# Performance work log

Hardware: AMD Instinct MI355X
Metric: run time of the kernel (lower is better)

The kernel has to match this reference:

```python
import jax, jax.numpy as jnp
import numpy as np

B, C_IN, L = 8, 12, 4096
D = 64        # mamba_in_ch
DI = 2 * D    # d_inner (expand=2)
DS = 16       # d_state
DC = 4        # d_conv
DTR = 4       # dt_rank = ceil(D/16)
R = 10        # pixel-shuffle / upsample factor
K = 15        # big conv kernel size

def _p(key, shape, scale=0.05):
    return (jax.random.normal(key, shape) * scale).astype(jnp.float32)

def setup_inputs() -> dict:
    key = jax.random.key(0)
    ks = jax.random.split(key, 12)
    return dict(
        x=jax.random.normal(ks[0], (B, C_IN, L), jnp.float32),
        conv_in_w=_p(ks[1], (D, C_IN, K)), conv_in_b=jnp.zeros((D,), jnp.float32),
        in_proj_w=_p(ks[2], (2 * DI, D)),
        dw_conv_w=_p(ks[3], (DI, 1, DC)), dw_conv_b=jnp.zeros((DI,), jnp.float32),
        x_proj_w=_p(ks[4], (DTR + 2 * DS, DI)),
        dt_proj_w=_p(ks[5], (DI, DTR)), dt_proj_b=_p(ks[6], (DI,)),
        A_log=jnp.log(jnp.tile(jnp.arange(1, DS + 1, dtype=jnp.float32)[None, :], (DI, 1))),
        D_ssm=jnp.ones((DI,), jnp.float32),
        out_proj_w=_p(ks[7], (D, DI)),
        conv_merge_w=_p(ks[8], (D, D, K)), conv_merge_b=jnp.zeros((D,), jnp.float32),
        bn_gamma=jnp.ones((D,), jnp.float32), bn_beta=jnp.zeros((D,), jnp.float32),
        conv_ps1_w=_p(ks[9], (R * C_IN, D, K)), conv_ps1_b=jnp.zeros((R * C_IN,), jnp.float32),
    )

def conv1d(x, w, b, pad_l, pad_r, groups=1):
    out = jax.lax.conv_general_dilated(x, w, (1,), [(pad_l, pad_r)],
        dimension_numbers=('NCH', 'OIH', 'NCH'), feature_group_count=groups)
    return out + b[None, :, None]

def mamba_layer(x, in_proj_w, dw_w, dw_b, x_proj_w, dt_proj_w, dt_proj_b, A_log, D_ssm, out_proj_w):
    # x: (B, L, D)
    xz = jnp.einsum('bld,ed->ble', x, in_proj_w)          # (B,L,2*DI)
    xs, z = jnp.split(xz, 2, axis=-1)
    xc = jnp.transpose(xs, (0, 2, 1))                      # (B,DI,L)
    xc = conv1d(xc, dw_w, dw_b, DC - 1, 0, groups=DI)      # causal depthwise conv, truncated to L
    xs = jax.nn.silu(jnp.transpose(xc, (0, 2, 1)))         # (B,L,DI)
    dbl = jnp.einsum('bld,ed->ble', xs, x_proj_w)          # (B,L,DTR+2*DS)
    dt, Bm, Cm = jnp.split(dbl, [DTR, DTR + DS], axis=-1)
    dt = jax.nn.softplus(jnp.einsum('blr,dr->bld', dt, dt_proj_w) + dt_proj_b)  # (B,L,DI)
    A = -jnp.exp(A_log)                                    # (DI,DS)
    dA = jnp.exp(dt[..., None] * A)                        # (B,L,DI,DS)
    dBx = dt[..., None] * Bm[:, :, None, :] * xs[..., None]

    def step(h, inputs):
        dA_t, dBx_t, C_t = inputs                          # (B,DI,DS),(B,DI,DS),(B,DS)
        h = dA_t * h + dBx_t
        y = jnp.einsum('bds,bs->bd', h, C_t)
        return h, y

    h0 = jnp.zeros((x.shape[0], DI, DS), x.dtype)
    _, ys = jax.lax.scan(step, h0,
        (jnp.transpose(dA, (1, 0, 2, 3)), jnp.transpose(dBx, (1, 0, 2, 3)), jnp.transpose(Cm, (1, 0, 2))))
    y = jnp.transpose(ys, (1, 0, 2)) + xs * D_ssm          # (B,L,DI)
    y = y * jax.nn.silu(z)
    return jnp.einsum('bld,ed->ble', y, out_proj_w)        # (B,L,D)

def reference(x, conv_in_w, conv_in_b, in_proj_w, dw_conv_w, dw_conv_b, x_proj_w,
              dt_proj_w, dt_proj_b, A_log, D_ssm, out_proj_w,
              conv_merge_w, conv_merge_b, bn_gamma, bn_beta, conv_ps1_w, conv_ps1_b):
    pad = (K - 1) // 2
    x_in = jax.nn.leaky_relu(conv1d(x, conv_in_w, conv_in_b, pad, pad), 0.01)  # (B,64,L)
    xm = jnp.transpose(x_in, (0, 2, 1))
    xm = xm + mamba_layer(xm, in_proj_w, dw_conv_w, dw_conv_b, x_proj_w,
                          dt_proj_w, dt_proj_b, A_log, D_ssm, out_proj_w)     # n_layer=1, residual
    xm = jnp.transpose(xm, (0, 2, 1))                                          # (B,64,L)
    xmerge = conv1d(xm, conv_merge_w, conv_merge_b, pad, pad)
    mean = jnp.mean(xmerge, axis=(0, 2), keepdims=True)                        # BatchNorm1d (training stats)
    var = jnp.var(xmerge, axis=(0, 2), keepdims=True)
    xmerge = (xmerge - mean) * jax.lax.rsqrt(var + 1e-5) * bn_gamma[None, :, None] + bn_beta[None, :, None]
    xmerge = xmerge + x_in
    xp = conv1d(xmerge, conv_ps1_w, conv_ps1_b, pad, pad)                      # (B,120,L)
    # PixelShuffle1D(r=10): (B, r*Cout, L) -> (B, Cout, L*r)
    Bn, ch, Ln = xp.shape
    ps = xp.reshape(Bn, R, ch // R, Ln).transpose(0, 2, 3, 1).reshape(Bn, ch // R, Ln * R)
    # F.interpolate(x, scale_factor=10, mode='linear', align_corners=False)
    out_len = L * R
    src = jnp.maximum((jnp.arange(out_len, dtype=jnp.float32) + 0.5) / R - 0.5, 0.0)
    i0 = jnp.minimum(jnp.floor(src).astype(jnp.int32), L - 1)
    i1 = jnp.minimum(i0 + 1, L - 1)
    frac = src - i0.astype(jnp.float32)
    up = x[..., i0] * (1.0 - frac) + x[..., i1] * frac
    return ps + up
```

## Files before the change

### kernel.cpp

```cpp
#include <hip/hip_runtime.h>
#include <math.h>

#define BB 8
#define CIN 12
#define LL 4096
#define DD 64
#define DIx 128
#define DSx 16
#define RR 10
#define KK 15
#define NCH 256
#define CLEN 16
#define OUTL 40960

typedef __attribute__((ext_vector_type(8))) short s8v;
typedef __attribute__((ext_vector_type(8))) __bf16 b8v;
typedef __attribute__((ext_vector_type(4))) float f4v;
union frag_u { s8v s; b8v b; };

__device__ __forceinline__ unsigned short f2b(float f) {
    unsigned int u = __float_as_uint(f);
    u = (u + 0x7fffu + ((u >> 16) & 1u)) >> 16;
    return (unsigned short)u;
}
__device__ __forceinline__ float b2f(unsigned short h) {
    return __uint_as_float(((unsigned int)h) << 16);
}

template<int CI, int CO, int COT, bool LEAKY>
__global__ __launch_bounds__(256) void k_conv(const float* __restrict__ in,
        const float* __restrict__ w, const float* __restrict__ bias,
        float* __restrict__ out) {
    const int LT = 1024;
    int tid = threadIdx.x;
    int bid = blockIdx.x;
    const int nlt = LL / LT;
    const int ncog = CO / COT;
    int lt = bid % nlt;
    int cog = (bid / nlt) % ncog;
    int b = bid / (nlt * ncog);
    int l0 = lt * LT + tid * 4;
    int co0 = cog * COT;

    float acc[COT][4];
#pragma unroll
    for (int c = 0; c < COT; ++c) {
        float bv = bias[co0 + c];
#pragma unroll
        for (int j = 0; j < 4; ++j) acc[c][j] = bv;
    }
    for (int ci = 0; ci < CI; ++ci) {
        const float* inp = in + ((size_t)b * CI + ci) * LL;
        float in20[20];
#pragma unroll
        for (int q = 0; q < 5; ++q) {
            int gi = l0 - 8 + q * 4;
            if (gi >= 0 && gi + 3 < LL) {
                float4 v = *(const float4*)(inp + gi);
                in20[q*4+0] = v.x; in20[q*4+1] = v.y;
                in20[q*4+2] = v.z; in20[q*4+3] = v.w;
            } else {
#pragma unroll
                for (int j = 0; j < 4; ++j) {
                    int g = gi + j;
                    in20[q*4+j] = (g >= 0 && g < LL) ? inp[g] : 0.f;
                }
            }
        }
#pragma unroll
        for (int c = 0; c < COT; ++c) {
            const float* wp = w + ((size_t)(co0 + c) * CI + ci) * KK;
#pragma unroll
            for (int k = 0; k < KK; ++k) {
                float wv = wp[k];
#pragma unroll
                for (int j = 0; j < 4; ++j)
                    acc[c][j] += wv * in20[j + k + 1];
            }
        }
    }
#pragma unroll
    for (int c = 0; c < COT; ++c) {
        float r[4];
#pragma unroll
        for (int j = 0; j < 4; ++j) {
            float v = acc[c][j];
            if (LEAKY) v = (v >= 0.f) ? v : 0.01f * v;
            r[j] = v;
        }
        *(float4*)(out + ((size_t)b * CO + co0 + c) * LL + l0) =
            make_float4(r[0], r[1], r[2], r[3]);
    }
}

template<int CO_REAL, int NCOB>
__global__ __launch_bounds__(256) void k_wprep(const float* __restrict__ w,
        unsigned short* __restrict__ wp) {
    int idx = blockIdx.x * 256 + threadIdx.x;
    if (idx >= 15 * NCOB * 1024) return;
    int j = idx & 7;
    int lane = (idx >> 3) & 63;
    int cis = (idx >> 9) & 1;
    int rest = idx >> 10;
    int cob = rest % NCOB;
    int kk = rest / NCOB;
    int co = cob * 16 + (lane & 15);
    int ci = cis * 32 + ((lane >> 4) << 3) + j;
    float val = (co < CO_REAL) ? w[((size_t)co * 64 + ci) * KK + kk] : 0.f;
    wp[idx] = f2b(val);
}

template<int CO_REAL, int NCOB>
__global__ __launch_bounds__(256) void k_convmfma(
        const unsigned short* __restrict__ xt,
        const unsigned short* __restrict__ wp,
        const float* __restrict__ bias, float* __restrict__ out) {
    __shared__ unsigned short in_lds[142 * 72];
    const int NCOT = NCOB / 4;
    int tid = threadIdx.x;
    int bid = blockIdx.x;
    int lt = bid & 31;
    int cot = (bid >> 5) % NCOT;
    int b = bid / (32 * NCOT);
    int l0 = lt * 128;
#pragma unroll
    for (int i = 0; i < 5; ++i) {
        int q = i * 256 + tid;
        if (q < 1136) {
            int r = q >> 3, c8 = (q & 7) * 8;
            int gl = l0 - 7 + r;
            s8v v = {0,0,0,0,0,0,0,0};
            if (gl >= 0 && gl < LL)
                v = *(const s8v*)&xt[((size_t)b * LL + gl) * 64 + c8];
            *(s8v*)&in_lds[r * 72 + c8] = v;
        }
    }
    __syncthreads();
    int lane = tid & 63, wv = tid >> 6;
    int corow = (lane >> 4) << 2;
    f4v acc[4][2];
#pragma unroll
    for (int mt = 0; mt < 4; ++mt) {
#pragma unroll
        for (int r = 0; r < 4; ++r) {
            int co = cot * 64 + mt * 16 + corow + r;
            float bv = (co < CO_REAL) ? bias[co] : 0.f;
            acc[mt][0][r] = bv;
            acc[mt][1][r] = bv;
        }
    }
    int bcol = lane & 15;
    int cig = (lane >> 4) << 3;
    for (int k = 0; k < KK; ++k) {
#pragma unroll
        for (int cis = 0; cis < 2; ++cis) {
            frag_u a[4], bf[2];
#pragma unroll
            for (int mt = 0; mt < 4; ++mt)
                a[mt].s = *(const s8v*)&wp[((((k * NCOB + cot * 4 + mt) * 2 + cis) << 9)
                                           + (lane << 3))];
#pragma unroll
            for (int nt = 0; nt < 2; ++nt)
                bf[nt].s = *(const s8v*)&in_lds[(wv * 32 + nt * 16 + bcol + k) * 72
                                               + cis * 32 + cig];
#pragma unroll
            for (int mt = 0; mt < 4; ++mt)
#pragma unroll
                for (int nt = 0; nt < 2; ++nt)
                    acc[mt][nt] = __builtin_amdgcn_mfma_f32_16x16x32_bf16(
                        a[mt].b, bf[nt].b, acc[mt][nt], 0, 0, 0);
        }
    }
#pragma unroll
    for (int mt = 0; mt < 4; ++mt)
#pragma unroll
        for (int nt = 0; nt < 2; ++nt) {
            int l = l0 + wv * 32 + nt * 16 + bcol;
#pragma unroll
            for (int r = 0; r < 4; ++r) {
                int co = cot * 64 + mt * 16 + corow + r;
                if (co < CO_REAL)
                    out[((size_t)b * CO_REAL + co) * LL + l] = acc[mt][nt][r];
            }
        }
}

__global__ __launch_bounds__(256) void k_gemm_inproj(const float* __restrict__ A,
        const float* __restrict__ W, float* __restrict__ C) {
    __shared__ float At[64 * 132];
    __shared__ float Wt[64 * 132];
    int tid = threadIdx.x;
    int bid = blockIdx.x;
    int nb = bid & 1;
    int mb = bid >> 1;
    int row0 = mb * 128;
    int n0 = nb * 128;
    int b = row0 >> 12;
    int l0 = row0 & 4095;
#pragma unroll
    for (int it = 0; it < 8; ++it) {
        int idx = it * 256 + tid;
        int k = idx >> 5, m4 = (idx & 31) * 4;
        float4 v = *(const float4*)(A + ((size_t)b * DD + k) * LL + l0 + m4);
        *(float4*)&At[k * 132 + m4] = v;
    }
#pragma unroll
    for (int it = 0; it < 8; ++it) {
        int lin = it * 1024 + tid * 4;
        int n = lin >> 6, k = lin & 63;
        float4 v = *(const float4*)(W + (size_t)(n0 + n) * 64 + k);
        Wt[(k+0)*132 + n] = v.x; Wt[(k+1)*132 + n] = v.y;
        Wt[(k+2)*132 + n] = v.z; Wt[(k+3)*132 + n] = v.w;
    }
    __syncthreads();
    int tx = tid & 15, ty = tid >> 4;
    float acc[2][2][4][4] = {};
#pragma unroll 4
    for (int k = 0; k < 64; ++k) {
        float4 aLo = *(float4*)&At[k*132 + ty*4];
        float4 aHi = *(float4*)&At[k*132 + 64 + ty*4];
        float4 bLo = *(float4*)&Wt[k*132 + tx*4];
        float4 bHi = *(float4*)&Wt[k*132 + 64 + tx*4];
        float a0[4] = {aLo.x, aLo.y, aLo.z, aLo.w};
        float a1[4] = {aHi.x, aHi.y, aHi.z, aHi.w};
        float b0[4] = {bLo.x, bLo.y, bLo.z, bLo.w};
        float b1[4] = {bHi.x, bHi.y, bHi.z, bHi.w};
#pragma unroll
        for (int mm = 0; mm < 4; ++mm)
#pragma unroll
            for (int nn = 0; nn < 4; ++nn) {
                acc[0][0][mm][nn] += a0[mm] * b0[nn];
                acc[0][1][mm][nn] += a0[mm] * b1[nn];
                acc[1][0][mm][nn] += a1[mm] * b0[nn];
                acc[1][1][mm][nn] += a1[mm] * b1[nn];
            }
    }
#pragma unroll
    for (int qm = 0; qm < 2; ++qm)
#pragma unroll
        for (int mm = 0; mm < 4; ++mm) {
            int row = row0 + qm*64 + ty*4 + mm;
#pragma unroll
            for (int qn = 0; qn < 2; ++qn) {
                float4 v = make_float4(acc[qm][qn][mm][0], acc[qm][qn][mm][1],
                                       acc[qm][qn][mm][2], acc[qm][qn][mm][3]);
                *(float4*)(C + (size_t)row * 256 + n0 + qn*64 + tx*4) = v;
            }
        }
}

template<int NW, bool GUARD>
__global__ __launch_bounds__(256) void k_gemm64(const float* __restrict__ A,
        const float* __restrict__ W, float* __restrict__ out) {
    __shared__ float At[64 * 132];
    __shared__ float Wt[64 * 68];
    int tid = threadIdx.x;
    int row0 = blockIdx.x * 128;
    int tx = tid & 15, ty = tid >> 4;
    float acc[2][4][4] = {};
#pragma unroll
    for (int kt = 0; kt < 2; ++kt) {
        __syncthreads();
#pragma unroll
        for (int it = 0; it < 8; ++it) {
            int lin = it * 1024 + tid * 4;
            int m = lin >> 6, k = lin & 63;
            float4 v = *(const float4*)(A + (size_t)(row0 + m) * 128 + kt*64 + k);
            At[(k+0)*132 + m] = v.x; At[(k+1)*132 + m] = v.y;
            At[(k+2)*132 + m] = v.z; At[(k+3)*132 + m] = v.w;
        }
#pragma unroll
        for (int it = 0; it < 4; ++it) {
            int lin = it * 1024 + tid * 4;
            int n = lin >> 6, k = lin & 63;
            float4 v = make_float4(0.f, 0.f, 0.f, 0.f);
            if (!GUARD || n < NW)
                v = *(const float4*)(W + (size_t)n * 128 + kt*64 + k);
            Wt[(k+0)*68 + n] = v.x; Wt[(k+1)*68 + n] = v.y;
            Wt[(k+2)*68 + n] = v.z; Wt[(k+3)*68 + n] = v.w;
        }
        __syncthreads();
#pragma unroll 4
        for (int k = 0; k < 64; ++k) {
            float4 aLo = *(float4*)&At[k*132 + ty*4];
            float4 aHi = *(float4*)&At[k*132 + 64 + ty*4];
            float4 b4  = *(float4*)&Wt[k*68 + tx*4];
            float a0[4] = {aLo.x, aLo.y, aLo.z, aLo.w};
            float a1[4] = {aHi.x, aHi.y, aHi.z, aHi.w};
            float bv[4] = {b4.x, b4.y, b4.z, b4.w};
#pragma unroll
            for (int mm = 0; mm < 4; ++mm)
#pragma unroll
                for (int nn = 0; nn < 4; ++nn) {
                    acc[0][mm][nn] += a0[mm] * bv[nn];
                    acc[1][mm][nn] += a1[mm] * bv[nn];
                }
        }
    }
#pragma unroll
    for (int qm = 0; qm < 2; ++qm)
#pragma unroll
        for (int mm = 0; mm < 4; ++mm) {
            int row = row0 + qm*64 + ty*4 + mm;
            *(float4*)(out + (size_t)row * 64 + tx*4) =
                make_float4(acc[qm][mm][0], acc[qm][mm][1],
                            acc[qm][mm][2], acc[qm][mm][3]);
        }
}

__global__ __launch_bounds__(256) void k_gemm64_tr(const float* __restrict__ A,
        const float* __restrict__ W, const float* __restrict__ res,
        unsigned short* __restrict__ out) {
    __shared__ float smem[13312];
    float* At = smem;
    float* Wt = smem + 64*132;
    int tid = threadIdx.x;
    int row0 = blockIdx.x * 128;
    int tx = tid & 15, ty = tid >> 4;
    int b = row0 >> 12, l0 = row0 & 4095;
    float acc[2][4][4] = {};
#pragma unroll
    for (int kt = 0; kt < 2; ++kt) {
        __syncthreads();
#pragma unroll
        for (int it = 0; it < 8; ++it) {
            int lin = it * 1024 + tid * 4;
            int m = lin >> 6, k = lin & 63;
            float4 v = *(const float4*)(A + (size_t)(row0 + m) * 128 + kt*64 + k);
            At[(k+0)*132 + m] = v.x; At[(k+1)*132 + m] = v.y;
            At[(k+2)*132 + m] = v.z; At[(k+3)*132 + m] = v.w;
        }
#pragma unroll
        for (int it = 0; it < 4; ++it) {
            int lin = it * 1024 + tid * 4;
            int n = lin >> 6, k = lin & 63;
            float4 v = *(const float4*)(W + (size_t)n * 128 + kt*64 + k);
            Wt[(k+0)*68 + n] = v.x; Wt[(k+1)*68 + n] = v.y;
            Wt[(k+2)*68 + n] = v.z; Wt[(k+3)*68 + n] = v.w;
        }
        __syncthreads();
#pragma unroll 4
        for (int k = 0; k < 64; ++k) {
            float4 aLo = *(float4*)&At[k*132 + ty*4];
            float4 aHi = *(float4*)&At[k*132 + 64 + ty*4];
            float4 b4  = *(float4*)&Wt[k*68 + tx*4];
            float a0[4] = {aLo.x, aLo.y, aLo.z, aLo.w};
            float a1[4] = {aHi.x, aHi.y, aHi.z, aHi.w};
            float bv[4] = {b4.x, b4.y, b4.z, b4.w};
#pragma unroll
            for (int mm = 0; mm < 4; ++mm)
#pragma unroll
                for (int nn = 0; nn < 4; ++nn) {
                    acc[0][mm][nn] += a0[mm] * bv[nn];
                    acc[1][mm][nn] += a1[mm] * bv[nn];
                }
        }
    }
    __syncthreads();
    float* tile = smem;
    unsigned short* resb = (unsigned short*)(smem + 8704);
#pragma unroll
    for (int qm = 0; qm < 2; ++qm)
#pragma unroll
        for (int mm = 0; mm < 4; ++mm) {
            int lrow = qm*64 + ty*4 + mm;
            *(float4*)&tile[lrow*68 + tx*4] = make_float4(
                acc[qm][mm][0], acc[qm][mm][1], acc[qm][mm][2], acc[qm][mm][3]);
        }
#pragma unroll
    for (int it = 0; it < 8; ++it) {
        int idx = it * 256 + tid;
        int d = idx >> 5, l4 = (idx & 31) * 4;
        float4 rv = *(const float4*)(res + ((size_t)b * DD + d) * LL + l0 + l4);
        resb[(l4+0)*72 + d] = f2b(rv.x);
        resb[(l4+1)*72 + d] = f2b(rv.y);
        resb[(l4+2)*72 + d] = f2b(rv.z);
        resb[(l4+3)*72 + d] = f2b(rv.w);
    }
    __syncthreads();
#pragma unroll
    for (int it = 0; it < 4; ++it) {
        int idx = it * 256 + tid;
        int l = idx >> 3, c8 = (idx & 7) * 8;
        unsigned short o[8];
#pragma unroll
        for (int j = 0; j < 8; ++j)
            o[j] = f2b(tile[l*68 + c8 + j] + b2f(resb[l*72 + c8 + j]));
        *(s8v*)&out[((size_t)b * LL + l0 + l) * 64 + c8] = *(s8v*)o;
    }
}

__global__ __launch_bounds__(256) void k_dwconv(const float* __restrict__ xz,
        const float* __restrict__ w, const float* __restrict__ bias,
        float* __restrict__ xs_act) {
    int idx = blockIdx.x * 256 + threadIdx.x;
    int d = idx & 127;
    int row = idx >> 7;
    int l = row & (LL - 1);
    float s = bias[d];
    const float* wp = w + d * 4;
#pragma unroll
    for (int j = 0; j < 4; ++j) {
        int li = l - 3 + j;
        if (li >= 0) s += xz[(size_t)(row - 3 + j) * 256 + d] * wp[j];
    }
    float sg = 1.f / (1.f + __expf(-s));
    xs_act[idx] = s * sg;
}

__global__ __launch_bounds__(256) void k_scan1(const float* __restrict__ xs,
        const float* __restrict__ dbl, const float* __restrict__ dtw,
        const float* __restrict__ dtbias, const float* __restrict__ A_log,
        float* __restrict__ P, float* __restrict__ Q) {
    __shared__ float sdbl[2][CLEN][64];
    int tid = threadIdx.x;
    int bid = blockIdx.x;
    int b = bid >> 7;
    int cpair = bid & 127;
    int half = tid >> 7;
    int d = tid & 127;
    int c = cpair * 2 + half;
    {
        const float4* src = (const float4*)(dbl +
            ((size_t)b * LL + (size_t)cpair * 2 * CLEN) * 64);
        float4* dst = (float4*)&sdbl[0][0][0];
        dst[tid] = src[tid];
        dst[256 + tid] = src[256 + tid];
    }
    __syncthreads();
    float4 w4 = *(const float4*)(dtw + d * 4);
    float dbias = dtbias[d];
    float Ads[16], h[16], p[16];
#pragma unroll
    for (int s = 0; s < 16; ++s) {
        Ads[s] = -__expf(A_log[d * DSx + s]);
        h[s] = 0.f; p[s] = 1.f;
    }
    size_t rowbase = (size_t)b * LL + (size_t)c * CLEN;
    const float* pxs = xs + rowbase * 128 + d;
    for (int t = 0; t < CLEN; ++t) {
        float4 di = *(const float4*)&sdbl[half][t][0];
        float dtv = di.x*w4.x + di.y*w4.y + di.z*w4.z + di.w*w4.w + dbias;
        dtv = (dtv > 15.f) ? dtv : log1pf(__expf(dtv));
        float xv = pxs[(size_t)t * 128];
        float dx = dtv * xv;
#pragma unroll
        for (int s = 0; s < 16; ++s) {
            float da = __expf(dtv * Ads[s]);
            h[s] = da * h[s] + dx * sdbl[half][t][4 + s];
            p[s] *= da;
        }
    }
    float* Pp = P + (size_t)c * 16384 + (size_t)(b * 128 + d) * 16;
    float* Qp = Q + (size_t)c * 16384 + (size_t)(b * 128 + d) * 16;
#pragma unroll
    for (int s4 = 0; s4 < 4; ++s4) {
        *(float4*)(Pp + s4*4) = make_float4(p[s4*4], p[s4*4+1], p[s4*4+2], p[s4*4+3]);
        *(float4*)(Qp + s4*4) = make_float4(h[s4*4], h[s4*4+1], h[s4*4+2], h[s4*4+3]);
    }
}

__global__ __launch_bounds__(256) void k_scan2(const float* __restrict__ P,
        const float* __restrict__ Q, float* __restrict__ Hin,
        float* __restrict__ stats) {
    int chain = blockIdx.x * 256 + threadIdx.x;
    if (blockIdx.x == 0 && threadIdx.x < 128) stats[threadIdx.x] = 0.f;
    float carry = 0.f;
    for (int c = 0; c < NCH; ++c) {
        Hin[(size_t)c * 16384 + chain] = carry;
        carry = P[(size_t)c * 16384 + chain] * carry + Q[(size_t)c * 16384 + chain];
    }
}

__global__ __launch_bounds__(256) void k_scan3(const float* __restrict__ xs,
        const float* __restrict__ dbl, const float* __restrict__ dtw,
        const float* __restrict__ dtbias, const float* __restrict__ A_log,
        const float* __restrict__ Hin, const float* __restrict__ xz,
        const float* __restrict__ Dssm, float* __restrict__ ym) {
    __shared__ float sdbl[2][CLEN][64];
    int tid = threadIdx.x;
    int bid = blockIdx.x;
    int b = bid >> 7;
    int cpair = bid & 127;
    int half = tid >> 7;
    int d = tid & 127;
    int c = cpair * 2 + half;
    {
        const float4* src = (const float4*)(dbl +
            ((size_t)b * LL + (size_t)cpair * 2 * CLEN) * 64);
        float4* dst = (float4*)&sdbl[0][0][0];
        dst[tid] = src[tid];
        dst[256 + tid] = src[256 + tid];
    }
    __syncthreads();
    float4 w4 = *(const float4*)(dtw + d * 4);
    float dbias = dtbias[d];
    float Dv = Dssm[d];
    float Ads[16], h[16];
#pragma unroll
    for (int s = 0; s < 16; ++s)
        Ads[s] = -__expf(A_log[d * DSx + s]);
    const float* Hp = Hin + (size_t)c * 16384 + (size_t)(b * 128 + d) * 16;
#pragma unroll
    for (int s4 = 0; s4 < 4; ++s4) {
        float4 hv = *(const float4*)(Hp + s4*4);
        h[s4*4+0] = hv.x; h[s4*4+1] = hv.y; h[s4*4+2] = hv.z; h[s4*4+3] = hv.w;
    }
    size_t rowbase = (size_t)b * LL + (size_t)c * CLEN;
    const float* pxs = xs + rowbase * 128 + d;
    const float* pz  = xz + rowbase * 256 + 128 + d;
    float* pym = ym + rowbase * 128 + d;
    for (int t = 0; t < CLEN; ++t) {
        float4 di = *(const float4*)&sdbl[half][t][0];
        float dtv = di.x*w4.x + di.y*w4.y + di.z*w4.z + di.w*w4.w + dbias;
        dtv = (dtv > 15.f) ? dtv : log1pf(__expf(dtv));
        float xv = pxs[(size_t)t * 128];
        float dx = dtv * xv;
        float y0 = 0.f, y1 = 0.f;
#pragma unroll
        for (int s = 0; s < 8; ++s) {
            float da = __expf(dtv * Ads[s]);
            h[s] = da * h[s] + dx * sdbl[half][t][4 + s];
            y0 += h[s] * sdbl[half][t][20 + s];
        }
#pragma unroll
        for (int s = 8; s < 16; ++s) {
            float da = __expf(dtv * Ads[s]);
            h[s] = da * h[s] + dx * sdbl[half][t][4 + s];
            y1 += h[s] * sdbl[half][t][20 + s];
        }
        float y = y0 + y1 + xv * Dv;
        float zv = pz[(size_t)t * 256];
        y *= zv / (1.f + __expf(-zv));
        pym[(size_t)t * 128] = y;
    }
}

__global__ __launch_bounds__(256) void k_bnpart(const float* __restrict__ xm,
        float* __restrict__ stats) {
    int c = blockIdx.x >> 3, b = blockIdx.x & 7;
    const float* p = xm + ((size_t)b * DD + c) * LL;
    int tid = threadIdx.x;
    float s = 0.f, ss = 0.f;
#pragma unroll
    for (int it = 0; it < 4; ++it) {
        float4 v = *(const float4*)(p + (size_t)(it * 256 + tid) * 4);
        s  += v.x + v.y + v.z + v.w;
        ss += v.x*v.x + v.y*v.y + v.z*v.z + v.w*v.w;
    }
    for (int o = 32; o > 0; o >>= 1) {
        s  += __shfl_down(s, o);
        ss += __shfl_down(ss, o);
    }
    __shared__ float red[8];
    int wid = tid >> 6;
    if ((tid & 63) == 0) { red[wid] = s; red[4 + wid] = ss; }
    __syncthreads();
    if (tid == 0) {
        atomicAdd(&stats[c], red[0] + red[1] + red[2] + red[3]);
        atomicAdd(&stats[64 + c], red[4] + red[5] + red[6] + red[7]);
    }
}

__global__ __launch_bounds__(256) void k_bnapply_t(const float* __restrict__ xm,
        const float* __restrict__ stats, const float* __restrict__ gamma,
        const float* __restrict__ beta, const float* __restrict__ xin,
        unsigned short* __restrict__ xf) {
    __shared__ float t[64][65];
    int tid = threadIdx.x;
    int b = blockIdx.x >> 6;
    int l0 = (blockIdx.x & 63) * 64;
    const float inv = 1.f / (float)(BB * LL);
#pragma unroll
    for (int it = 0; it < 16; ++it) {
        int idx = it * 256 + tid;
        int c = idx >> 6, l = idx & 63;
        float mean = stats[c] * inv;
        float var  = stats[64 + c] * inv - mean * mean;
        float g = gamma[c] * rsqrtf(var + 1e-5f);
        float sh = beta[c] - mean * g;
        size_t addr = ((size_t)b * DD + c) * LL + l0 + l;
        t[c][l] = xm[addr] * g + sh + xin[addr];
    }
    __syncthreads();
#pragma unroll
    for (int it = 0; it < 2; ++it) {
        int idx = it * 256 + tid;
        int l = idx >> 3, c8 = (idx & 7) * 8;
        unsigned short o[8];
#pragma unroll
        for (int j = 0; j < 8; ++j) o[j] = f2b(t[c8 + j][l]);
        *(s8v*)&xf[((size_t)b * LL + l0 + l) * 64 + c8] = *(s8v*)o;
    }
}

__global__ __launch_bounds__(256) void k_final(const float* __restrict__ xp,
        const float* __restrict__ x, float* __restrict__ out) {
    __shared__ float xps[10][257];
    __shared__ float xr[258];
    int tid = threadIdx.x;
    int bid = blockIdx.x;
    int lt = bid & 15;
    int c = (bid >> 4) % 12;
    int b = bid / (16 * 12);
    int l0 = lt * 256;
#pragma unroll
    for (int r = 0; r < 10; ++r)
        xps[r][tid] = xp[((size_t)b * 120 + r * 12 + c) * LL + l0 + tid];
    const float* xrow = x + ((size_t)b * 12 + c) * LL;
    for (int i = tid; i < 258; i += 256) {
        int g = l0 - 1 + i;
        g = (g < 0) ? 0 : ((g > LL - 1) ? LL - 1 : g);
        xr[i] = xrow[g];
    }
    __syncthreads();
    size_t obase = ((size_t)b * 12 + c) * OUTL + (size_t)l0 * 10;
#pragma unroll
    for (int u = 0; u < 10; ++u) {
        int j = u * 256 + tid;
        int jg = l0 * 10 + j;
        int l = j / 10, r = j - l * 10;
        float ps = xps[r][l];
        float src = ((float)jg + 0.5f) * 0.1f - 0.5f;
        src = fmaxf(src, 0.f);
        int i0 = (int)src;
        if (i0 > LL - 1) i0 = LL - 1;
        int i1 = (i0 + 1 < LL) ? i0 + 1 : LL - 1;
        float frac = src - (float)i0;
        float up = xr[i0 - l0 + 1] * (1.f - frac) + xr[i1 - l0 + 1] * frac;
        out[obase + j] = ps + up;
    }
}

extern "C" void kernel_launch(void* const* d_in, const int* in_sizes, int n_in,
                              void* d_out, int out_size, void* d_ws, size_t ws_size,
                              hipStream_t stream) {
    const float* x          = (const float*)d_in[0];
    const float* conv_in_w  = (const float*)d_in[1];
    const float* conv_in_b  = (const float*)d_in[2];
    const float* in_proj_w  = (const float*)d_in[3];
    const float* dw_w       = (const float*)d_in[4];
    const float* dw_b       = (const float*)d_in[5];
    const float* x_proj_w   = (const float*)d_in[6];
    const float* dt_w       = (const float*)d_in[7];
    const float* dt_b       = (const float*)d_in[8];
    const float* A_log      = (const float*)d_in[9];
    const float* Dssm       = (const float*)d_in[10];
    const float* out_proj_w = (const float*)d_in[11];
    const float* cm_w       = (const float*)d_in[12];
    const float* cm_b       = (const float*)d_in[13];
    const float* bn_g       = (const float*)d_in[14];
    const float* bn_be      = (const float*)d_in[15];
    const float* ps_w       = (const float*)d_in[16];
    const float* ps_b       = (const float*)d_in[17];

    float* ws = (float*)d_ws;
    float* xin_bdl = ws;
    float* xz      = ws + 2097152;
    float* xs_act  = ws + 10485760;
    float* dbl64   = ws + 14680064;
    float* P       = ws + 16777216;
    float* Q       = ws + 20971520;
    float* Hin     = ws + 25165824;
    float* stats   = ws + 29360128;
    float* ym      = P;
    float* xmerge  = dbl64;
    unsigned short* xmt = (unsigned short*)(ws + 10485760);
    unsigned short* xf  = (unsigned short*)(ws + 11534336);
    unsigned short* wp_ps = (unsigned short*)(ws + 6029312);
    unsigned short* wp_mg = (unsigned short*)(ws + 6090752);
    float* xp      = xz;

    k_conv<CIN, 64, 2, true><<<1024, 256, 0, stream>>>(x, conv_in_w, conv_in_b, xin_bdl);
    k_gemm_inproj<<<512, 256, 0, stream>>>(xin_bdl, in_proj_w, xz);
    k_dwconv<<<16384, 256, 0, stream>>>(xz, dw_w, dw_b, xs_act);
    k_gemm64<36, true><<<256, 256, 0, stream>>>(xs_act, x_proj_w, dbl64);
    k_scan1<<<1024, 256, 0, stream>>>(xs_act, dbl64, dt_w, dt_b, A_log, P, Q);
    k_scan2<<<64, 256, 0, stream>>>(P, Q, Hin, stats);
    k_scan3<<<1024, 256, 0, stream>>>(xs_act, dbl64, dt_w, dt_b, A_log, Hin, xz, Dssm, ym);
    k_wprep<120, 8><<<480, 256, 0, stream>>>(ps_w, wp_ps);
    k_wprep<64, 4><<<240, 256, 0, stream>>>(cm_w, wp_mg);
    k_gemm64_tr<<<256, 256, 0, stream>>>(ym, out_proj_w, xin_bdl, xmt);
    k_convmfma<64, 4><<<256, 256, 0, stream>>>(xmt, wp_mg, cm_b, xmerge);
    k_bnpart<<<512, 256, 0, stream>>>(xmerge, stats);
    k_bnapply_t<<<512, 256, 0, stream>>>(xmerge, stats, bn_g, bn_be, xin_bdl, xf);
    k_convmfma<120, 8><<<512, 256, 0, stream>>>(xf, wp_ps, ps_b, xp);
    k_final<<<1536, 256, 0, stream>>>(xp, x, (float*)d_out);
}
```

Before: 343.8 us.

## Fuse depthwise conv into consumers, store intermediates as bf16, fuse BN stats

Removes the standalone depthwise-conv kernel by recomputing the causal conv plus SiLU inside the x_proj GEMM and both scan kernels, reading a bf16 copy of the in_proj output. Intermediates (xz, ym, the pixel-shuffle conv output) are stored as bf16 to cut memory traffic. BatchNorm partial sums are computed in the merge conv epilogue with shuffles and atomics, replacing the separate reduction kernel. The scan chunk count is halved with longer chunks. This adds recomputation and bf16 rounding error in activations in exchange for fewer passes over global memory.

Measured after the change: 425.8 us. +23.8%, slower.

```diff
diff --git a/kernel.cpp b/kernel.cpp
--- a/kernel.cpp
+++ b/kernel.cpp
@@ -9,8 +9,8 @@
 #define DSx 16
 #define RR 10
 #define KK 15
-#define NCH 256
-#define CLEN 16
+#define NCH 128
+#define CLEN 32
 #define OUTL 40960
 
 typedef __attribute__((ext_vector_type(8))) short s8v;
@@ -110,11 +110,12 @@
     wp[idx] = f2b(val);
 }
 
-template<int CO_REAL, int NCOB>
+template<int CO_REAL, int NCOB, int MODE>
 __global__ __launch_bounds__(256) void k_convmfma(
         const unsigned short* __restrict__ xt,
         const unsigned short* __restrict__ wp,
-        const float* __restrict__ bias, float* __restrict__ out) {
+        const float* __restrict__ bias, void* __restrict__ outv,
+        float* __restrict__ stats) {
     __shared__ unsigned short in_lds[142 * 72];
     const int NCOT = NCOB / 4;
     int tid = threadIdx.x;
@@ -179,14 +180,38 @@
 #pragma unroll
             for (int r = 0; r < 4; ++r) {
                 int co = cot * 64 + mt * 16 + corow + r;
-                if (co < CO_REAL)
-                    out[((size_t)b * CO_REAL + co) * LL + l] = acc[mt][nt][r];
+                if (co < CO_REAL) {
+                    if (MODE == 0)
+                        ((float*)outv)[((size_t)b * CO_REAL + co) * LL + l] = acc[mt][nt][r];
+                    else
+                        ((unsigned short*)outv)[((size_t)b * CO_REAL + co) * LL + l]
+                            = f2b(acc[mt][nt][r]);
+                }
             }
         }
+    if (MODE == 0) {
+#pragma unroll
+        for (int mt = 0; mt < 4; ++mt)
+#pragma unroll
+            for (int r = 0; r < 4; ++r) {
+                float sv = acc[mt][0][r] + acc[mt][1][r];
+                float ssv = acc[mt][0][r]*acc[mt][0][r] + acc[mt][1][r]*acc[mt][1][r];
+#pragma unroll
+                for (int off = 1; off < 16; off <<= 1) {
+                    sv  += __shfl_xor(sv, off);
+                    ssv += __shfl_xor(ssv, off);
+                }
+                if (bcol == 0) {
+                    int co = mt * 16 + corow + r;
+                    atomicAdd(&stats[co], sv);
+                    atomicAdd(&stats[64 + co], ssv);
+                }
+            }
+    }
 }
 
 __global__ __launch_bounds__(256) void k_gemm_inproj(const float* __restrict__ A,
-        const float* __restrict__ W, float* __restrict__ C) {
+        const float* __restrict__ W, unsigned short* __restrict__ C) {
     __shared__ float At[64 * 132];
     __shared__ float Wt[64 * 132];
     int tid = threadIdx.x;
@@ -242,39 +267,65 @@
             int row = row0 + qm*64 + ty*4 + mm;
 #pragma unroll
             for (int qn = 0; qn < 2; ++qn) {
-                float4 v = make_float4(acc[qm][qn][mm][0], acc[qm][qn][mm][1],
-                                       acc[qm][qn][mm][2], acc[qm][qn][mm][3]);
-                *(float4*)(C + (size_t)row * 256 + n0 + qn*64 + tx*4) = v;
+                unsigned short o[4];
+#pragma unroll
+                for (int nn = 0; nn < 4; ++nn) o[nn] = f2b(acc[qm][qn][mm][nn]);
+                *(uint2*)&C[(size_t)row * 256 + n0 + qn*64 + tx*4] = *(uint2*)o;
             }
         }
 }
 
-template<int NW, bool GUARD>
-__global__ __launch_bounds__(256) void k_gemm64(const float* __restrict__ A,
+template<int NW>
+__global__ __launch_bounds__(256) void k_gemm64dw(
+        const unsigned short* __restrict__ xzb,
+        const float* __restrict__ dww, const float* __restrict__ dwb,
         const float* __restrict__ W, float* __restrict__ out) {
     __shared__ float At[64 * 132];
     __shared__ float Wt[64 * 68];
+    __shared__ float sdw[128][4];
+    __shared__ float sbias[128];
     int tid = threadIdx.x;
     int row0 = blockIdx.x * 128;
+    int l0 = row0 & 4095;
+    if (tid < 128) {
+        *(float4*)&sdw[tid][0] = *(const float4*)(dww + tid * 4);
+        sbias[tid] = dwb[tid];
+    }
     int tx = tid & 15, ty = tid >> 4;
     float acc[2][4][4] = {};
 #pragma unroll
     for (int kt = 0; kt < 2; ++kt) {
         __syncthreads();
 #pragma unroll
-        for (int it = 0; it < 8; ++it) {
-            int lin = it * 1024 + tid * 4;
-            int m = lin >> 6, k = lin & 63;
-            float4 v = *(const float4*)(A + (size_t)(row0 + m) * 128 + kt*64 + k);
-            At[(k+0)*132 + m] = v.x; At[(k+1)*132 + m] = v.y;
-            At[(k+2)*132 + m] = v.z; At[(k+3)*132 + m] = v.w;
+        for (int it = 0; it < 4; ++it) {
+            int task = it * 256 + tid;
+            int m = task >> 3;
+            int k8 = (task & 7) * 8;
+            int d0 = kt * 64 + k8;
+            float s[8];
+#pragma unroll
+            for (int j = 0; j < 8; ++j) s[j] = sbias[d0 + j];
+#pragma unroll
+            for (int tap = 0; tap < 4; ++tap) {
+                if (l0 + m - 3 + tap >= 0) {
+                    s8v xv = *(const s8v*)&xzb[(size_t)(row0 + m - 3 + tap) * 256 + d0];
+#pragma unroll
+                    for (int j = 0; j < 8; ++j)
+                        s[j] += b2f((unsigned short)xv[j]) * sdw[d0 + j][tap];
+                }
+            }
+#pragma unroll
+            for (int j = 0; j < 8; ++j) {
+                float v = s[j];
+                At[(k8 + j) * 132 + m] = v / (1.f + __expf(-v));
+            }
         }
 #pragma unroll
         for (int it = 0; it < 4; ++it) {
             int lin = it * 1024 + tid * 4;
             int n = lin >> 6, k = lin & 63;
             float4 v = make_float4(0.f, 0.f, 0.f, 0.f);
-            if (!GUARD || n < NW)
+            if (n < NW)
                 v = *(const float4*)(W + (size_t)n * 128 + kt*64 + k);
             Wt[(k+0)*68 + n] = v.x; Wt[(k+1)*68 + n] = v.y;
             Wt[(k+2)*68 + n] = v.z; Wt[(k+3)*68 + n] = v.w;
@@ -308,9 +359,9 @@
         }
 }
 
-__global__ __launch_bounds__(256) void k_gemm64_tr(const float* __restrict__ A,
-        const float* __restrict__ W, const float* __restrict__ res,
-        unsigned short* __restrict__ out) {
+__global__ __launch_bounds__(256) void k_gemm64_tr(
+        const unsigned short* __restrict__ A, const float* __restrict__ W,
+        const float* __restrict__ res, unsigned short* __restrict__ out) {
     __shared__ float smem[13312];
     float* At = smem;
     float* Wt = smem + 64*132;
@@ -323,12 +374,14 @@
     for (int kt = 0; kt < 2; ++kt) {
         __syncthreads();
 #pragma unroll
-        for (int it = 0; it < 8; ++it) {
-            int lin = it * 1024 + tid * 4;
-            int m = lin >> 6, k = lin & 63;
-            float4 v = *(const float4*)(A + (size_t)(row0 + m) * 128 + kt*64 + k);
-            At[(k+0)*132 + m] = v.x; At[(k+1)*132 + m] = v.y;
-            At[(k+2)*132 + m] = v.z; At[(k+3)*132 + m] = v.w;
+        for (int it = 0; it < 4; ++it) {
+            int task = it * 256 + tid;
+            int m = task >> 3;
+            int k8 = (task & 7) * 8;
+            s8v v = *(const s8v*)&A[(size_t)(row0 + m) * 128 + kt*64 + k8];
+#pragma unroll
+            for (int j = 0; j < 8; ++j)
+                At[(k8 + j) * 132 + m] = b2f((unsigned short)v[j]);
         }
 #pragma unroll
         for (int it = 0; it < 4; ++it) {
@@ -390,33 +443,17 @@
     }
 }
 
-__global__ __launch_bounds__(256) void k_dwconv(const float* __restrict__ xz,
-        const float* __restrict__ w, const float* __restrict__ bias,
-        float* __restrict__ xs_act) {
-    int idx = blockIdx.x * 256 + threadIdx.x;
-    int d = idx & 127;
-    int row = idx >> 7;
-    int l = row & (LL - 1);
-    float s = bias[d];
-    const float* wp = w + d * 4;
-#pragma unroll
-    for (int j = 0; j < 4; ++j) {
-        int li = l - 3 + j;
-        if (li >= 0) s += xz[(size_t)(row - 3 + j) * 256 + d] * wp[j];
-    }
-    float sg = 1.f / (1.f + __expf(-s));
-    xs_act[idx] = s * sg;
-}
-
-__global__ __launch_bounds__(256) void k_scan1(const float* __restrict__ xs,
-        const float* __restrict__ dbl, const float* __restrict__ dtw,
-        const float* __restrict__ dtbias, const float* __restrict__ A_log,
-        float* __restrict__ P, float* __restrict__ Q) {
+__global__ __launch_bounds__(256) void k_scan1(
+        const unsigned short* __restrict__ xzb, const float* __restrict__ dbl,
+        const float* __restrict__ dww, const float* __restrict__ dwb,
+        const float* __restrict__ dtw, const float* __restrict__ dtbias,
+        const float* __restrict__ A_log, float* __restrict__ P,
+        float* __restrict__ Q) {
     __shared__ float sdbl[2][CLEN][64];
     int tid = threadIdx.x;
     int bid = blockIdx.x;
-    int b = bid >> 7;
-    int cpair = bid & 127;
+    int b = bid >> 6;
+    int cpair = bid & 63;
     int half = tid >> 7;
     int d = tid & 127;
     int c = cpair * 2 + half;
@@ -424,26 +461,33 @@
         const float4* src = (const float4*)(dbl +
             ((size_t)b * LL + (size_t)cpair * 2 * CLEN) * 64);
         float4* dst = (float4*)&sdbl[0][0][0];
-        dst[tid] = src[tid];
-        dst[256 + tid] = src[256 + tid];
+#pragma unroll
+        for (int i = 0; i < 4; ++i) dst[i * 256 + tid] = src[i * 256 + tid];
     }
     __syncthreads();
     float4 w4 = *(const float4*)(dtw + d * 4);
     float dbias = dtbias[d];
+    float4 cw = *(const float4*)(dww + d * 4);
+    float cbias = dwb[d];
     float Ads[16], h[16], p[16];
 #pragma unroll
     for (int s = 0; s < 16; ++s) {
         Ads[s] = -__expf(A_log[d * DSx + s]);
         h[s] = 0.f; p[s] = 1.f;
     }
-    size_t rowbase = (size_t)b * LL + (size_t)c * CLEN;
-    const float* pxs = xs + rowbase * 128 + d;
+    int l0 = c * CLEN;
+    const unsigned short* px = xzb + ((size_t)b * LL + l0) * 256 + d;
+    float w0 = 0.f, w1 = 0.f, w2 = 0.f;
+    if (l0) { w0 = b2f(px[-768]); w1 = b2f(px[-512]); w2 = b2f(px[-256]); }
     for (int t = 0; t < CLEN; ++t) {
+        float cur = b2f(px[(size_t)t * 256]);
+        float sv = cbias + w0*cw.x + w1*cw.y + w2*cw.z + cur*cw.w;
+        float xs = sv / (1.f + __expf(-sv));
+        w0 = w1; w1 = w2; w2 = cur;
         float4 di = *(const float4*)&sdbl[half][t][0];
         float dtv = di.x*w4.x + di.y*w4.y + di.z*w4.z + di.w*w4.w + dbias;
         dtv = (dtv > 15.f) ? dtv : log1pf(__expf(dtv));
-        float xv = pxs[(size_t)t * 128];
-        float dx = dtv * xv;
+        float dx = dtv * xs;
 #pragma unroll
         for (int s = 0; s < 16; ++s) {
             float da = __expf(dtv * Ads[s]);
@@ -472,16 +516,17 @@
     }
 }
 
-__global__ __launch_bounds__(256) void k_scan3(const float* __restrict__ xs,
-        const float* __restrict__ dbl, const float* __restrict__ dtw,
-        const float* __restrict__ dtbias, const float* __restrict__ A_log,
-        const float* __restrict__ Hin, const float* __restrict__ xz,
-        const float* __restrict__ Dssm, float* __restrict__ ym) {
+__global__ __launch_bounds__(256) void k_scan3(
+        const unsigned short* __restrict__ xzb, const float* __restrict__ dbl,
+        const float* __restrict__ dww, const float* __restrict__ dwb,
+        const float* __restrict__ dtw, const float* __restrict__ dtbias,
+        const float* __restrict__ A_log, const float* __restrict__ Hin,
+        const float* __restrict__ Dssm, unsigned short* __restrict__ ymb) {
     __shared__ float sdbl[2][CLEN][64];
     int tid = threadIdx.x;
     int bid = blockIdx.x;
-    int b = bid >> 7;
-    int cpair = bid & 127;
+    int b = bid >> 6;
+    int cpair = bid & 63;
     int half = tid >> 7;
     int d = tid & 127;
     int c = cpair * 2 + half;
@@ -489,12 +534,14 @@
         const float4* src = (const float4*)(dbl +
             ((size_t)b * LL + (size_t)cpair * 2 * CLEN) * 64);
         float4* dst = (float4*)&sdbl[0][0][0];
-        dst[tid] = src[tid];
-        dst[256 + tid] = src[256 + tid];
+#pragma unroll
+        for (int i = 0; i < 4; ++i) dst[i * 256 + tid] = src[i * 256 + tid];
     }
     __syncthreads();
     float4 w4 = *(const float4*)(dtw + d * 4);
     float dbias = dtbias[d];
+    float4 cw = *(const float4*)(dww + d * 4);
+    float cbias = dwb[d];
     float Dv = Dssm[d];
     float Ads[16], h[16];
 #pragma unroll
@@ -506,16 +553,22 @@
         float4 hv = *(const float4*)(Hp + s4*4);
         h[s4*4+0] = hv.x; h[s4*4+1] = hv.y; h[s4*4+2] = hv.z; h[s4*4+3] = hv.w;
     }
-    size_t rowbase = (size_t)b * LL + (size_t)c * CLEN;
-    const float* pxs = xs + rowbase * 128 + d;
-    const float* pz  = xz + rowbase * 256 + 128 + d;
-    float* pym = ym + rowbase * 128 + d;
+    int l0 = c * CLEN;
+    size_t rowbase = (size_t)b * LL + l0;
+    const unsigned short* px = xzb + rowbase * 256 + d;
+    const unsigned short* pz = xzb + rowbase * 256 + 128 + d;
+    unsigned short* pym = ymb + rowbase * 128 + d;
+    float w0 = 0.f, w1 = 0.f, w2 = 0.f;
+    if (l0) { w0 = b2f(px[-768]); w1 = b2f(px[-512]); w2 = b2f(px[-256]); }
     for (int t = 0; t < CLEN; ++t) {
+        float cur = b2f(px[(size_t)t * 256]);
+        float sv = cbias + w0*cw.x + w1*cw.y + w2*cw.z + cur*cw.w;
+        float xs = sv / (1.f + __expf(-sv));
+        w0 = w1; w1 = w2; w2 = cur;
         float4 di = *(const float4*)&sdbl[half][t][0];
         float dtv = di.x*w4.x + di.y*w4.y + di.z*w4.z + di.w*w4.w + dbias;
         dtv = (dtv > 15.f) ? dtv : log1pf(__expf(dtv));
-        float xv = pxs[(size_t)t * 128];
-        float dx = dtv * xv;
+        float dx = dtv * xs;
         float y0 = 0.f, y1 = 0.f;
 #pragma unroll
         for (int s = 0; s < 8; ++s) {
@@ -529,36 +582,10 @@
             h[s] = da * h[s] + dx * sdbl[half][t][4 + s];
             y1 += h[s] * sdbl[half][t][20 + s];
         }
-        float y = y0 + y1 + xv * Dv;
-        float zv = pz[(size_t)t * 256];
+        float y = y0 + y1 + xs * Dv;
+        float zv = b2f(pz[(size_t)t * 256]);
         y *= zv / (1.f + __expf(-zv));
-        pym[(size_t)t * 128] = y;
-    }
-}
-
-__global__ __launch_bounds__(256) void k_bnpart(const float* __restrict__ xm,
-        float* __restrict__ stats) {
-    int c = blockIdx.x >> 3, b = blockIdx.x & 7;
-    const float* p = xm + ((size_t)b * DD + c) * LL;
-    int tid = threadIdx.x;
-    float s = 0.f, ss = 0.f;
-#pragma unroll
-    for (int it = 0; it < 4; ++it) {
-        float4 v = *(const float4*)(p + (size_t)(it * 256 + tid) * 4);
-        s  += v.x + v.y + v.z + v.w;
-        ss += v.x*v.x + v.y*v.y + v.z*v.z + v.w*v.w;
-    }
-    for (int o = 32; o > 0; o >>= 1) {
-        s  += __shfl_down(s, o);
-        ss += __shfl_down(ss, o);
-    }
-    __shared__ float red[8];
-    int wid = tid >> 6;
-    if ((tid & 63) == 0) { red[wid] = s; red[4 + wid] = ss; }
-    __syncthreads();
-    if (tid == 0) {
-        atomicAdd(&stats[c], red[0] + red[1] + red[2] + red[3]);
-        atomicAdd(&stats[64 + c], red[4] + red[5] + red[6] + red[7]);
+        pym[(size_t)t * 128] = f2b(y);
     }
 }
 
@@ -594,7 +621,7 @@
     }
 }
 
-__global__ __launch_bounds__(256) void k_final(const float* __restrict__ xp,
+__global__ __launch_bounds__(256) void k_final(const unsigned short* __restrict__ xp,
         const float* __restrict__ x, float* __restrict__ out) {
     __shared__ float xps[10][257];
     __shared__ float xr[258];
@@ -606,7 +633,7 @@
     int l0 = lt * 256;
 #pragma unroll
     for (int r = 0; r < 10; ++r)
-        xps[r][tid] = xp[((size_t)b * 120 + r * 12 + c) * LL + l0 + tid];
+        xps[r][tid] = b2f(xp[((size_t)b * 120 + r * 12 + c) * LL + l0 + tid]);
     const float* xrow = x + ((size_t)b * 12 + c) * LL;
     for (int i = tid; i < 258; i += 256) {
         int g = l0 - 1 + i;
@@ -656,34 +683,32 @@
 
     float* ws = (float*)d_ws;
     float* xin_bdl = ws;
-    float* xz      = ws + 2097152;
-    float* xs_act  = ws + 10485760;
-    float* dbl64   = ws + 14680064;
-    float* P       = ws + 16777216;
-    float* Q       = ws + 20971520;
-    float* Hin     = ws + 25165824;
-    float* stats   = ws + 29360128;
-    float* ym      = P;
-    float* xmerge  = dbl64;
-    unsigned short* xmt = (unsigned short*)(ws + 10485760);
-    unsigned short* xf  = (unsigned short*)(ws + 11534336);
-    unsigned short* wp_ps = (unsigned short*)(ws + 6029312);
-    unsigned short* wp_mg = (unsigned short*)(ws + 6090752);
-    float* xp      = xz;
+    unsigned short* xzb = (unsigned short*)(ws + 2097152);
+    float* dbl64   = ws + 6291456;
+    float* P       = ws + 8388608;
+    float* Q       = ws + 10485760;
+    float* Hin     = ws + 12582912;
+    float* stats   = ws + 14680064;
+    unsigned short* ymb = (unsigned short*)(ws + 14680192);
+    unsigned short* xmt = (unsigned short*)(ws + 16777344);
+    float* xmerge  = ws + 17825920;
+    unsigned short* xf  = (unsigned short*)(ws + 19923072);
+    unsigned short* wp_ps = (unsigned short*)(ws + 20971648);
+    unsigned short* wp_mg = (unsigned short*)(ws + 21033088);
+    unsigned short* xpb = (unsigned short*)(ws + 21063808);
 
     k_conv<CIN, 64, 2, true><<<1024, 256, 0, stream>>>(x, conv_in_w, conv_in_b, xin_bdl);
-    k_gemm_inproj<<<512, 256, 0, stream>>>(xin_bdl, in_proj_w, xz);
-    k_dwconv<<<16384, 256, 0, stream>>>(xz, dw_w, dw_b, xs_act);
-    k_gemm64<36, true><<<256, 256, 0, stream>>>(xs_act, x_proj_w, dbl64);
-    k_scan1<<<1024, 256, 0, stream>>>(xs_act, dbl64, dt_w, dt_b, A_log, P, Q);
+    k_gemm_inproj<<<512, 256, 0, stream>>>(xin_bdl, in_proj_w, xzb);
+    k_gemm64dw<36><<<256, 256, 0, stream>>>(xzb, dw_w, dw_b, x_proj_w, dbl64);
+    k_scan1<<<512, 256, 0, stream>>>(xzb, dbl64, dw_w, dw_b, dt_w, dt_b, A_log, P, Q);
     k_scan2<<<64, 256, 0, stream>>>(P, Q, Hin, stats);
-    k_scan3<<<1024, 256, 0, stream>>>(xs_act, dbl64, dt_w, dt_b, A_log, Hin, xz, Dssm, ym);
+    k_scan3<<<512, 256, 0, stream>>>(xzb, dbl64, dw_w, dw_b, dt_w, dt_b, A_log, Hin,
+                                     Dssm, ymb);
     k_wprep<120, 8><<<480, 256, 0, stream>>>(ps_w, wp_ps);
     k_wprep<64, 4><<<240, 256, 0, stream>>>(cm_w, wp_mg);
-    k_gemm64_tr<<<256, 256, 0, stream>>>(ym, out_proj_w, xin_bdl, xmt);
-    k_convmfma<64, 4><<<256, 256, 0, stream>>>(xmt, wp_mg, cm_b, xmerge);
-    k_bnpart<<<512, 256, 0, stream>>>(xmerge, stats);
+    k_gemm64_tr<<<256, 256, 0, stream>>>(ymb, out_proj_w, xin_bdl, xmt);
+    k_convmfma<64, 4, 0><<<256, 256, 0, stream>>>(xmt, wp_mg, cm_b, xmerge, stats);
     k_bnapply_t<<<512, 256, 0, stream>>>(xmerge, stats, bn_g, bn_be, xin_bdl, xf);
-    k_convmfma<120, 8><<<512, 256, 0, stream>>>(xf, wp_ps, ps_b, xp);
-    k_final<<<1536, 256, 0, stream>>>(xp, x, (float*)d_out);
-}
+    k_convmfma<120, 8, 1><<<512, 256, 0, stream>>>(xf, wp_ps, ps_b, xpb, nullptr);
+    k_final<<<1536, 256, 0, stream>>>(xpb, x, (float*)d_out);
+}
```
